# Performance work log

Hardware: AMD Instinct MI355X
Metric: run time of the kernel (lower is better)

Reference implementation:

```python
import jax, jax.numpy as jnp
import numpy as np

B, T, C = 2, 2048, 1024
H = 16
D = C // H  # head_dim = 64
EPS = 1e-06
MAX_SEQ = 2048


def make_rotary(dim, max_seq_len, base=10000):
    inv_freq = 1.0 / (base ** (jnp.arange(0, dim, 2, dtype=jnp.float32) / dim))
    pos = jnp.arange(max_seq_len, dtype=jnp.float32)
    sinusoid = jnp.einsum('i,j->ij', pos, inv_freq)  # (S, dim//2)
    return jnp.sin(sinusoid), jnp.cos(sinusoid)


def apply_rotary(x, sin, cos):
    # x: (B, T, H, D); sin/cos: (MAX_SEQ, D//2)
    t = x.shape[1]
    s = sin[:t][:, None, :]  # (T,1,D//2) broadcasts over B and H
    c = cos[:t][:, None, :]
    d = x.shape[-1]
    x1, x2 = x[..., :d // 2], x[..., d // 2:]
    return jnp.concatenate([x1 * c - x2 * s, x2 * c + x1 * s], axis=-1)


def yat_dense(x, kernel, bias, alpha, eps=EPS):
    # Yat layer: squared dot product over squared euclidean distance.
    dot = x @ kernel                                   # (..., out)
    x_sq = jnp.sum(x * x, axis=-1, keepdims=True)      # (..., 1)
    k_sq = jnp.sum(kernel * kernel, axis=0)            # (out,)
    dist = x_sq + k_sq - 2.0 * dot
    y = (dot * dot) / (dist + eps)
    out_f = kernel.shape[1]
    scale = (jnp.sqrt(jnp.float32(out_f)) / jnp.log(1.0 + jnp.float32(out_f))) ** alpha
    return y * scale + bias


def setup_inputs() -> dict:
    key = jax.random.key(0)
    ks = jax.random.split(key, 7)
    x = jax.random.normal(ks[0], (B, T, C), dtype=jnp.float32)
    mask = jnp.tril(jnp.ones((T, T), dtype=bool))[None].repeat(B, axis=0)  # (B,T,T) causal
    s = 1.0 / np.sqrt(C)
    w_attn = jax.random.normal(ks[1], (C, 3 * C), dtype=jnp.float32) * s
    b_attn = jnp.zeros((3 * C,), dtype=jnp.float32)
    a_attn = jnp.ones((1,), dtype=jnp.float32)
    w_proj = jax.random.normal(ks[2], (C, C), dtype=jnp.float32) * s
    b_proj = jnp.zeros((C,), dtype=jnp.float32)
    a_proj = jnp.ones((1,), dtype=jnp.float32)
    return {"x": x, "mask": mask, "w_attn": w_attn, "b_attn": b_attn,
            "a_attn": a_attn, "w_proj": w_proj, "b_proj": b_proj, "a_proj": a_proj}


def reference(x, mask, w_attn, b_attn, a_attn, w_proj, b_proj, a_proj):
    b, t, c = x.shape
    sin, cos = make_rotary(D, MAX_SEQ)
    qkv = yat_dense(x, w_attn, b_attn, a_attn)          # (B,T,3C)
    qkv = qkv.reshape(b, t, 3, H, D)
    q, k, v = jnp.moveaxis(qkv, 2, 0)                   # each (B,T,H,D)
    q = apply_rotary(q, sin, cos)
    k = apply_rotary(k, sin, cos)
    # heads-major layout for attention
    q = q.transpose(0, 2, 1, 3)                          # (B,H,T,D)
    k = k.transpose(0, 2, 1, 3)
    v = v.transpose(0, 2, 1, 3)
    scale = jnp.sqrt(jnp.float32(D))
    attn = jnp.einsum('bhqd,bhkd->bhqk', q, k) / scale   # (B,H,T,T)
    m = mask[:, None, :, :]                              # (B,1,T,T)
    attn = jnp.where(m, attn, jnp.finfo(jnp.float32).min)
    attn = jax.nn.softmax(attn, axis=-1)
    # dropout is identity in deterministic/eval mode
    out = jnp.einsum('bhqk,bhkd->bhqd', attn, v)         # (B,H,T,D)
    out = out.transpose(0, 2, 1, 3).reshape(b, t, c)     # (B,T,C)
    out = yat_dense(out, w_proj, b_proj, a_proj)
    return out
```

## Files before the change

### kernel.cpp

```cpp
#include <hip/hip_runtime.h>
#include <math.h>

#define TSEQ  2048
#define BATCH 2
#define NH    16
#define HD    64
#define CDIM  1024
#define N3C   3072
#define EPSY  1e-6f

typedef unsigned short u16;
typedef unsigned int u32;
typedef __attribute__((ext_vector_type(2))) unsigned int u32x2;
typedef __attribute__((ext_vector_type(8))) short bf16x8;
typedef __attribute__((ext_vector_type(4))) float f32x4;

#define MFMA16(a, b, c) __builtin_amdgcn_mfma_f32_16x16x32_bf16(a, b, c, 0, 0, 0)

__device__ __forceinline__ u16 f2bf(float f) {
    unsigned u = __float_as_uint(f);
    return (u16)((u + 0x7fffu + ((u >> 16) & 1u)) >> 16);
}
__device__ __forceinline__ u32 cvtpk_bf16(float lo, float hi) {
    u32 r;
    asm("v_cvt_pk_bf16_f32 %0, %1, %2" : "=v"(r) : "v"(lo), "v"(hi));
    return r;
}
__device__ __forceinline__ void gload16(const void* g, void* l) {
    __builtin_amdgcn_global_load_lds(
        (const __attribute__((address_space(1))) unsigned int*)g,
        (__attribute__((address_space(3))) unsigned int*)l, 16, 0, 0);
}

__global__ __launch_bounds__(256) void prep_kernel(
    const float* __restrict__ x, const float* __restrict__ wa,
    const float* __restrict__ wp, u16* __restrict__ Ahi,
    u16* __restrict__ Wthi, u16* __restrict__ Wphi,
    float* __restrict__ ksq, float* __restrict__ xsq,
    float* __restrict__ osq, float2* __restrict__ ropeSC) {
    __shared__ float smem[64 * 68];
    int bid = blockIdx.x, tid = threadIdx.x;

    if (bid < 4096) {
        int lane = tid & 63, wv = tid >> 6;
        size_t base = (size_t)bid * CDIM + tid * 4;
        float4 v = *(const float4*)(x + base);
        ushort4 hi;
        hi.x = f2bf(v.x); hi.y = f2bf(v.y); hi.z = f2bf(v.z); hi.w = f2bf(v.w);
        *(ushort4*)(Ahi + base) = hi;
        float s = v.x * v.x + v.y * v.y + v.z * v.z + v.w * v.w;
        #pragma unroll
        for (int off = 32; off; off >>= 1) s += __shfl_down(s, off, 64);
        if (lane == 0) smem[wv] = s;
        __syncthreads();
        if (tid == 0) xsq[bid] = smem[0] + smem[1] + smem[2] + smem[3];
    } else if (bid < 5120) {
        const float* W; u16* Whi; int K, N, bx, by;
        if (bid < 4864) {
            int t = bid - 4096; W = wa; Whi = Wthi; K = CDIM; N = N3C;
            bx = t % 48; by = t / 48;
        } else {
            int t = bid - 4864; W = wp; Whi = Wphi; K = CDIM; N = CDIM;
            bx = t % 16; by = t / 16;
        }
        int k0 = by * 64, n0 = bx * 64;
        int r = tid >> 4, c4 = (tid & 15) * 4;
        #pragma unroll
        for (int i = 0; i < 4; ++i) {
            int k = k0 + r + i * 16;
            float4 v = *(const float4*)(W + (size_t)k * N + n0 + c4);
            *(float4*)&smem[(r + i * 16) * 68 + c4] = v;
        }
        __syncthreads();
        int n = tid >> 4, k4 = (tid & 15) * 4;
        #pragma unroll
        for (int i = 0; i < 4; ++i) {
            int nn = n + i * 16;
            ushort4 hi;
            hi.x = f2bf(smem[(k4 + 0) * 68 + nn]);
            hi.y = f2bf(smem[(k4 + 1) * 68 + nn]);
            hi.z = f2bf(smem[(k4 + 2) * 68 + nn]);
            hi.w = f2bf(smem[(k4 + 3) * 68 + nn]);
            *(ushort4*)(Whi + (size_t)(n0 + nn) * K + k0 + k4) = hi;
        }
    } else if (bid < 5184) {
        int b2 = bid - 5120;
        int c = tid & 63, kq = tid >> 6;
        const float* W; int N, col, outoff;
        if (b2 < 48) { W = wa; N = N3C;  col = b2 * 64 + c;        outoff = 0;   }
        else         { W = wp; N = CDIM; col = (b2 - 48) * 64 + c; outoff = N3C; }
        float s = 0.f;
        int i0 = kq * 256;
        #pragma unroll 4
        for (int i = i0; i < i0 + 256; ++i) {
            float v = W[(size_t)i * N + col];
            s = fmaf(v, v, s);
        }
        smem[tid] = s;
        __syncthreads();
        if (kq == 0)
            ksq[outoff + col] = smem[c] + smem[64 + c] + smem[128 + c] + smem[192 + c];
    } else {
        int idx = (bid - 5184) * 256 + tid;
        if (idx < BATCH * TSEQ) osq[idx] = 0.f;
        int t = idx >> 5, j = idx & 31;
        float inv = exp2f(-(float)j * 0.4152410118609203f);
        float ang = (float)t * inv;
        ropeSC[idx] = make_float2(cosf(ang), sinf(ang));
    }
}

__global__ __launch_bounds__(256, 4) void gemm1_fused(
    const u16* __restrict__ Ah, const u16* __restrict__ Bh,
    const float* __restrict__ bias, const float* __restrict__ rowsq,
    const float* __restrict__ colsq, const float* __restrict__ alphap,
    const float2* __restrict__ ropeSC,
    u16* __restrict__ Qb, u16* __restrict__ Kb, u16* __restrict__ Vt) {
    constexpr int BK = 32;
    const int K = CDIM;
    __shared__ u16 Ash[2][128 * BK], Bsh[2][128 * BK];
    int tid = threadIdx.x;
    int lane = tid & 63, wv = tid >> 6;
    int quad = lane >> 4, l15 = lane & 15;
    int wr = wv >> 1, wc = wv & 1;

    int lin = blockIdx.x + blockIdx.y * 24;
    int swz = (lin & 7) * 96 + (lin >> 3);
    int bn = (swz % 24) * 128;
    int bm = (swz / 24) * 128;

    int rsub = lane >> 2;
    int lc8 = (lane & 3) * 8;
    int gc8 = (((lane & 3) - (rsub >> 1)) & 3) * 8;
    int pf8 = ((quad + (l15 >> 1)) & 3) * 8;

    f32x4 acc[4][4];
    #pragma unroll
    for (int i = 0; i < 4; ++i)
        #pragma unroll
        for (int j = 0; j < 4; ++j) acc[i][j] = (f32x4){0.f, 0.f, 0.f, 0.f};

    auto STAGE = [&](int buf, int kt) {
        #pragma unroll
        for (int i = 0; i < 2; ++i) {
            int r = i * 64 + wv * 16 + rsub;
            gload16(Ah + (size_t)(bm + r) * K + kt + gc8, &Ash[buf][r * BK + lc8]);
            gload16(Bh + (size_t)(bn + r) * K + kt + gc8, &Bsh[buf][r * BK + lc8]);
        }
    };

    STAGE(0, 0);
    __syncthreads();
    int cur = 0;

    for (int kt = 0; kt < K; kt += BK) {
        if (kt + BK < K) STAGE(cur ^ 1, kt + BK);
        bf16x8 fah[4], fbh[4];
        #pragma unroll
        for (int i = 0; i < 4; ++i)
            fah[i] = *(const bf16x8*)&Ash[cur][(wr * 64 + i * 16 + l15) * BK + pf8];
        #pragma unroll
        for (int j = 0; j < 4; ++j)
            fbh[j] = *(const bf16x8*)&Bsh[cur][(wc * 64 + j * 16 + l15) * BK + pf8];
        #pragma unroll
        for (int i = 0; i < 4; ++i)
            #pragma unroll
            for (int j = 0; j < 4; ++j)
                acc[i][j] = MFMA16(fah[i], fbh[j], acc[i][j]);
        __syncthreads();
        cur ^= 1;
    }

    float alpha = alphap[0];
    float scale = powf(sqrtf((float)N3C) / logf(1.0f + (float)N3C), alpha);
    int segc0 = bn + wc * 64;
    int seg = segc0 >> 10;
    int h = (segc0 >> 6) & 15;
    int bglob = bm >> 11;
    int bh = bglob * NH + h;

    if (seg < 2) {
        u16* dst = (seg == 0) ? Qb : Kb;
        float qs = (seg == 0) ? 0.18033688011112043f : 1.0f;
        #pragma unroll
        for (int i = 0; i < 4; ++i) {
            int tb = bm + wr * 64 + i * 16 + quad * 4;
            #pragma unroll
            for (int r = 0; r < 4; ++r) {
                int row = tb + r;
                int t = row & (TSEQ - 1);
                float rs = rowsq[row];
                float y[4];
                #pragma unroll
                for (int j = 0; j < 4; ++j) {
                    int col = segc0 + j * 16 + l15;
                    float dot = acc[i][j][r];
                    float dist = rs + colsq[col] - 2.0f * dot + EPSY;
                    y[j] = dot * dot / dist * scale + bias[col];
                }
                float2 sc0 = ropeSC[t * 32 + l15];
                float2 sc1 = ropeSC[t * 32 + 16 + l15];
                float c0 = sc0.x, s0 = sc0.y, c1 = sc1.x, s1 = sc1.y;
                size_t ob = ((size_t)bh * TSEQ + t) * HD;
                dst[ob + l15]      = f2bf((y[0] * c0 - y[2] * s0) * qs);
                dst[ob + 16 + l15] = f2bf((y[1] * c1 - y[3] * s1) * qs);
                dst[ob + 32 + l15] = f2bf((y[2] * c0 + y[0] * s0) * qs);
                dst[ob + 48 + l15] = f2bf((y[3] * c1 + y[1] * s1) * qs);
            }
        }
    } else {
        #pragma unroll
        for (int i = 0; i < 4; ++i) {
            int tb = bm + wr * 64 + i * 16 + quad * 4;
            int t0 = tb & (TSEQ - 1);
            #pragma unroll
            for (int j = 0; j < 4; ++j) {
                int col = segc0 + j * 16 + l15;
                int d = j * 16 + l15;
                float cs = colsq[col], bi = bias[col];
                ushort4 pk;
                u16* pp = (u16*)&pk;
                #pragma unroll
                for (int r = 0; r < 4; ++r) {
                    float dot = acc[i][j][r];
                    float dist = rowsq[tb + r] + cs - 2.0f * dot + EPSY;
                    pp[r] = f2bf(dot * dot / dist * scale + bi);
                }
                *(ushort4*)(Vt + ((size_t)bh * HD + d) * TSEQ + t0) = pk;
            }
        }
    }
}

__global__ __launch_bounds__(128, 4) void gemm_yat_mfma(
    const u16* __restrict__ Ah, const u16* __restrict__ Bh,
    const float* __restrict__ bias, const float* __restrict__ rowsq,
    const float* __restrict__ colsq, const float* __restrict__ alphap,
    float* __restrict__ outp, int M, int N, int K, float outf) {
    constexpr int BM = 64, BN = 64, BK = 32;
    __shared__ u16 Ash[2][BM * BK], Bsh[2][BN * BK];
    int tid = threadIdx.x;
    int lane = tid & 63, wv = tid >> 6;
    int quad = lane >> 4, l15 = lane & 15;

    int lin = blockIdx.x + blockIdx.y * 16;
    int swz = (lin & 7) * 128 + (lin >> 3);
    int bn = (swz & 15) * BN;
    int bm = (swz >> 4) * BM;

    int rs = tid >> 2;
    int cc = tid & 3;
    int lc8 = cc * 8;
    int gc8 = ((cc - ((rs & 15) >> 1)) & 3) * 8;
    int pf8 = ((quad + (l15 >> 1)) & 3) * 8;

    f32x4 acc[2][4];
    #pragma unroll
    for (int i = 0; i < 2; ++i)
        #pragma unroll
        for (int j = 0; j < 4; ++j) acc[i][j] = (f32x4){0.f, 0.f, 0.f, 0.f};

    auto STAGE = [&](int buf, int kt) {
        #pragma unroll
        for (int p = 0; p < 2; ++p) {
            int r = p * 32 + rs;
            gload16(Ah + (size_t)(bm + r) * K + kt + gc8, &Ash[buf][r * BK + lc8]);
            gload16(Bh + (size_t)(bn + r) * K + kt + gc8, &Bsh[buf][r * BK + lc8]);
        }
    };

    STAGE(0, 0);
    __syncthreads();
    int cur = 0;

    for (int kt = 0; kt < K; kt += BK) {
        if (kt + BK < K) STAGE(cur ^ 1, kt + BK);
        bf16x8 fah[2], fbh[4];
        #pragma unroll
        for (int i = 0; i < 2; ++i)
            fah[i] = *(const bf16x8*)&Ash[cur][(wv * 32 + i * 16 + l15) * BK + pf8];
        #pragma unroll
        for (int j = 0; j < 4; ++j)
            fbh[j] = *(const bf16x8*)&Bsh[cur][(j * 16 + l15) * BK + pf8];
        #pragma unroll
        for (int i = 0; i < 2; ++i)
            #pragma unroll
            for (int j = 0; j < 4; ++j)
                acc[i][j] = MFMA16(fah[i], fbh[j], acc[i][j]);
        __syncthreads();
        cur ^= 1;
    }

    float alpha = alphap[0];
    float scale = powf(sqrtf(outf) / logf(1.0f + outf), alpha);
    #pragma unroll
    for (int j = 0; j < 4; ++j) {
        int col = bn + j * 16 + l15;
        float cs = colsq[col], bi = bias[col];
        #pragma unroll
        for (int i = 0; i < 2; ++i) {
            #pragma unroll
            for (int r = 0; r < 4; ++r) {
                int row = bm + wv * 32 + i * 16 + quad * 4 + r;
                float dot = acc[i][j][r];
                float dist = rowsq[row] + cs - 2.0f * dot + EPSY;
                outp[(size_t)row * N + col] = dot * dot / dist * scale + bi;
            }
        }
    }
}

__global__ __launch_bounds__(512) void attn_mfma(
    const u16* __restrict__ Qb, const u16* __restrict__ Kb,
    const u16* __restrict__ Vt, u16* __restrict__ Chi,
    float* __restrict__ osq) {
    __shared__ u16 Ksh[2][64 * 64];
    __shared__ u16 Vsh[2][64 * 64];
    int tid = threadIdx.x;
    int lane = tid & 63, wv = tid >> 6;
    int quad = lane >> 4, l15 = lane & 15;
    const bool oddq = (quad & 1) != 0;
    int bh = blockIdx.x;
    int b = bh >> 4, h = bh & 15;
    const u16* Qh = Qb + (size_t)bh * TSEQ * HD;
    const u16* Kh = Kb + (size_t)bh * TSEQ * HD;
    const u16* Vh = Vt + (size_t)bh * HD * TSEQ;
    const f32x4 zf = {0.f, 0.f, 0.f, 0.f};

    int qbb = 15 - blockIdx.y;
    int qw = qbb * 128 + wv * 16;
    int NT = 2 * qbb + 2;
    bf16x8 bq0 = *(const bf16x8*)(Qh + (size_t)(qw + l15) * HD + quad * 8);
    bf16x8 bq1 = *(const bf16x8*)(Qh + (size_t)(qw + l15) * HD + 32 + quad * 8);

    f32x4 o[4] = {zf, zf, zf, zf};
    float l = 0.f;

    auto STAGE = [&](int buf, int kt) {
        int k0s = kt * 64;
        int rowi = tid >> 3, ch = tid & 7;
        int gk = (ch + rowi) & 7;
        gload16(Kh + (size_t)(k0s + rowi) * HD + gk * 8, &Ksh[buf][tid * 8]);
        gload16(Vh + (size_t)rowi * TSEQ + k0s + gk * 8, &Vsh[buf][tid * 8]);
    };

    STAGE(0, 0);
    __syncthreads();
    int cur = 0;

    for (int kt = 0; kt < NT; ++kt) {
        int k0 = kt * 64;
        if (kt + 1 < NT) STAGE(cur ^ 1, kt + 1);
        if (k0 <= qw + 15) {
            const u16* Kc = Ksh[cur];
            const u16* Vc = Vsh[cur];

            f32x4 st[4];
            __builtin_amdgcn_s_setprio(1);
            #pragma unroll
            for (int mt = 0; mt < 4; ++mt) {
                int key = mt * 16 + l15;
                bf16x8 a0 = *(const bf16x8*)&Kc[key * 64 + ((quad - key) & 7) * 8];
                bf16x8 a1 = *(const bf16x8*)&Kc[key * 64 + ((4 + quad - key) & 7) * 8];
                st[mt] = MFMA16(a0, bq0, zf);
                st[mt] = MFMA16(a1, bq1, st[mt]);
            }
            __builtin_amdgcn_s_setprio(0);
            if (k0 + 63 > qw) {
                int q = qw + l15;
                #pragma unroll
                for (int mt = 0; mt < 4; ++mt)
                    #pragma unroll
                    for (int r = 0; r < 4; ++r)
                        if (k0 + mt * 16 + quad * 4 + r > q) st[mt][r] = -1e30f;
            }
            u32 pp[4][2];
            #pragma unroll
            for (int mt = 0; mt < 4; ++mt) {
                float p0 = __builtin_amdgcn_exp2f(st[mt][0]);
                float p1 = __builtin_amdgcn_exp2f(st[mt][1]);
                float p2 = __builtin_amdgcn_exp2f(st[mt][2]);
                float p3 = __builtin_amdgcn_exp2f(st[mt][3]);
                l += (p0 + p1) + (p2 + p3);
                pp[mt][0] = cvtpk_bf16(p0, p1);
                pp[mt][1] = cvtpk_bf16(p2, p3);
            }
            #pragma unroll
            for (int s = 0; s < 2; ++s) {
                u32x2 r0 = __builtin_amdgcn_permlane32_swap(
                    pp[2 * s][0], pp[2 * s + 1][0], false, false);
                u32 sA0 = (u32)__builtin_amdgcn_ds_swizzle((int)r0.x, 0x401F);
                u32 sB0 = (u32)__builtin_amdgcn_ds_swizzle((int)r0.y, 0x401F);
                u32x2 r1 = __builtin_amdgcn_permlane32_swap(
                    pp[2 * s][1], pp[2 * s + 1][1], false, false);
                u32 sA1 = (u32)__builtin_amdgcn_ds_swizzle((int)r1.x, 0x401F);
                u32 sB1 = (u32)__builtin_amdgcn_ds_swizzle((int)r1.y, 0x401F);
                u32 bw0 = oddq ? sB0 : r0.x;
                u32 bw1 = oddq ? sB1 : r1.x;
                u32 bw2 = oddq ? r0.y : sA0;
                u32 bw3 = oddq ? r1.y : sA1;
                bf16x8 bfr;
                *(u32*)&((short*)&bfr)[0] = bw0;
                *(u32*)&((short*)&bfr)[2] = bw1;
                *(u32*)&((short*)&bfr)[4] = bw2;
                *(u32*)&((short*)&bfr)[6] = bw3;
                __builtin_amdgcn_s_setprio(1);
                #pragma unroll
                for (int dt = 0; dt < 4; ++dt) {
                    int d = dt * 16 + l15;
                    bf16x8 av = *(const bf16x8*)&Vc[d * 64 + ((s * 4 + quad - d) & 7) * 8];
                    o[dt] = MFMA16(av, bfr, o[dt]);
                }
                __builtin_amdgcn_s_setprio(0);
            }
        }
        __syncthreads();
        cur ^= 1;
    }

    l += __shfl_xor(l, 16, 64);
    l += __shfl_xor(l, 32, 64);
    float inv = 1.0f / l;
    int row = (b << 11) + qw + l15;
    float ss = 0.f;
    #pragma unroll
    for (int dt = 0; dt < 4; ++dt) {
        float v0 = o[dt][0] * inv, v1 = o[dt][1] * inv;
        float v2 = o[dt][2] * inv, v3 = o[dt][3] * inv;
        ss += v0 * v0 + v1 * v1 + v2 * v2 + v3 * v3;
        uint2 pk2;
        pk2.x = cvtpk_bf16(v0, v1);
        pk2.y = cvtpk_bf16(v2, v3);
        *(uint2*)(Chi + (size_t)row * CDIM + h * HD + dt * 16 + quad * 4) = pk2;
    }
    ss += __shfl_xor(ss, 16, 64);
    ss += __shfl_xor(ss, 32, 64);
    if (quad == 0) atomicAdd(osq + row, ss);
}

extern "C" void kernel_launch(void* const* d_in, const int* in_sizes, int n_in,
                              void* d_out, int out_size, void* d_ws, size_t ws_size,
                              hipStream_t stream) {
    const float* x      = (const float*)d_in[0];
    const float* w_attn = (const float*)d_in[2];
    const float* b_attn = (const float*)d_in[3];
    const float* a_attn = (const float*)d_in[4];
    const float* w_proj = (const float*)d_in[5];
    const float* b_proj = (const float*)d_in[6];
    const float* a_proj = (const float*)d_in[7];
    float* outp = (float*)d_out;

    char* ws = (char*)d_ws;
    float* ksq = (float*)(ws);
    float* xsq = (float*)(ws + 16384);
    float* osq = (float*)(ws + 32768);
    char* pA  = ws + 65536;
    u16* Ahi = (u16*)pA;
    u16* Chi = (u16*)pA;
    char* pWt = pA + 16777216;
    u16* Wthi = (u16*)pWt;
    char* pWp = pWt + 6291456;
    u16* Wphi = (u16*)pWp;
    char* pQ = pWp + 2097152;
    u16* Qb = (u16*)pQ;
    u16* Kb = (u16*)(pQ + 8388608);
    u16* Vt = (u16*)(pQ + 16777216);
    float2* ropeSC = (float2*)(pQ + 25165824);

    prep_kernel<<<5440, 256, 0, stream>>>(
        x, w_attn, w_proj, Ahi, Wthi, Wphi, ksq, xsq, osq, ropeSC);
    gemm1_fused<<<dim3(N3C / 128, (BATCH * TSEQ) / 128), 256, 0, stream>>>(
        Ahi, Wthi, b_attn, xsq, ksq, a_attn, ropeSC, Qb, Kb, Vt);
    attn_mfma<<<dim3(BATCH * NH, 16), 512, 0, stream>>>(Qb, Kb, Vt, Chi, osq);
    gemm_yat_mfma<<<dim3(CDIM / 64, (BATCH * TSEQ) / 64), 128, 0, stream>>>(
        Chi, Wphi, b_proj, osq, ksq + N3C, a_proj, outp,
        BATCH * TSEQ, CDIM, CDIM, (float)CDIM);
}
```

Measured before the change: 222.8 us.

## Drop LDS staging in attention, read K/V directly from global memory

The attention kernel no longer stages K and V tiles through double-buffered shared memory with block-wide barriers. Each wave now loads its MFMA operands for K and V straight from global memory, relying on L1/L2 caches. Blocks shrink from 8 waves covering 128 query rows to 4 waves covering 64 rows, and the grid doubles so causal work is spread more finely. This removes the barriers and the LDS traffic, but each wave now fetches K/V on its own with uncoalesced, cache-dependent loads and loses cross-wave reuse.

```diff
diff --git a/kernel.cpp b/kernel.cpp
--- a/kernel.cpp
+++ b/kernel.cpp
@@ -310,12 +310,10 @@
     }
 }
 
-__global__ __launch_bounds__(512) void attn_mfma(
+__global__ __launch_bounds__(256) void attn_mfma(
     const u16* __restrict__ Qb, const u16* __restrict__ Kb,
     const u16* __restrict__ Vt, u16* __restrict__ Chi,
     float* __restrict__ osq) {
-    __shared__ u16 Ksh[2][64 * 64];
-    __shared__ u16 Vsh[2][64 * 64];
     int tid = threadIdx.x;
     int lane = tid & 63, wv = tid >> 6;
     int quad = lane >> 4, l15 = lane & 15;
@@ -327,95 +325,78 @@
     const u16* Vh = Vt + (size_t)bh * HD * TSEQ;
     const f32x4 zf = {0.f, 0.f, 0.f, 0.f};
 
-    int qbb = 15 - blockIdx.y;
-    int qw = qbb * 128 + wv * 16;
-    int NT = 2 * qbb + 2;
+    int qblk = 31 - blockIdx.y;
+    int qw = qblk * 64 + wv * 16;
+    int NT = qblk + 1;
     bf16x8 bq0 = *(const bf16x8*)(Qh + (size_t)(qw + l15) * HD + quad * 8);
     bf16x8 bq1 = *(const bf16x8*)(Qh + (size_t)(qw + l15) * HD + 32 + quad * 8);
 
     f32x4 o[4] = {zf, zf, zf, zf};
     float l = 0.f;
 
-    auto STAGE = [&](int buf, int kt) {
-        int k0s = kt * 64;
-        int rowi = tid >> 3, ch = tid & 7;
-        int gk = (ch + rowi) & 7;
-        gload16(Kh + (size_t)(k0s + rowi) * HD + gk * 8, &Ksh[buf][tid * 8]);
-        gload16(Vh + (size_t)rowi * TSEQ + k0s + gk * 8, &Vsh[buf][tid * 8]);
-    };
-
-    STAGE(0, 0);
-    __syncthreads();
-    int cur = 0;
-
     for (int kt = 0; kt < NT; ++kt) {
         int k0 = kt * 64;
-        if (kt + 1 < NT) STAGE(cur ^ 1, kt + 1);
-        if (k0 <= qw + 15) {
-            const u16* Kc = Ksh[cur];
-            const u16* Vc = Vsh[cur];
-
-            f32x4 st[4];
+        if (k0 > qw + 15) continue;
+
+        f32x4 st[4];
+        __builtin_amdgcn_s_setprio(1);
+        #pragma unroll
+        for (int mt = 0; mt < 4; ++mt) {
+            int key = k0 + mt * 16 + l15;
+            const u16* kr = Kh + (size_t)key * HD;
+            bf16x8 a0 = *(const bf16x8*)(kr + quad * 8);
+            bf16x8 a1 = *(const bf16x8*)(kr + 32 + quad * 8);
+            st[mt] = MFMA16(a0, bq0, zf);
+            st[mt] = MFMA16(a1, bq1, st[mt]);
+        }
+        __builtin_amdgcn_s_setprio(0);
+        if (k0 + 63 > qw) {
+            int q = qw + l15;
+            #pragma unroll
+            for (int mt = 0; mt < 4; ++mt)
+                #pragma unroll
+                for (int r = 0; r < 4; ++r)
+                    if (k0 + mt * 16 + quad * 4 + r > q) st[mt][r] = -1e30f;
+        }
+        u32 pp[4][2];
+        #pragma unroll
+        for (int mt = 0; mt < 4; ++mt) {
+            float p0 = __builtin_amdgcn_exp2f(st[mt][0]);
+            float p1 = __builtin_amdgcn_exp2f(st[mt][1]);
+            float p2 = __builtin_amdgcn_exp2f(st[mt][2]);
+            float p3 = __builtin_amdgcn_exp2f(st[mt][3]);
+            l += (p0 + p1) + (p2 + p3);
+            pp[mt][0] = cvtpk_bf16(p0, p1);
+            pp[mt][1] = cvtpk_bf16(p2, p3);
+        }
+        #pragma unroll
+        for (int s = 0; s < 2; ++s) {
+            u32x2 r0 = __builtin_amdgcn_permlane32_swap(
+                pp[2 * s][0], pp[2 * s + 1][0], false, false);
+            u32 sA0 = (u32)__builtin_amdgcn_ds_swizzle((int)r0.x, 0x401F);
+            u32 sB0 = (u32)__builtin_amdgcn_ds_swizzle((int)r0.y, 0x401F);
+            u32x2 r1 = __builtin_amdgcn_permlane32_swap(
+                pp[2 * s][1], pp[2 * s + 1][1], false, false);
+            u32 sA1 = (u32)__builtin_amdgcn_ds_swizzle((int)r1.x, 0x401F);
+            u32 sB1 = (u32)__builtin_amdgcn_ds_swizzle((int)r1.y, 0x401F);
+            u32 bw0 = oddq ? sB0 : r0.x;
+            u32 bw1 = oddq ? sB1 : r1.x;
+            u32 bw2 = oddq ? r0.y : sA0;
+            u32 bw3 = oddq ? r1.y : sA1;
+            bf16x8 bfr;
+            *(u32*)&((short*)&bfr)[0] = bw0;
+            *(u32*)&((short*)&bfr)[2] = bw1;
+            *(u32*)&((short*)&bfr)[4] = bw2;
+            *(u32*)&((short*)&bfr)[6] = bw3;
             __builtin_amdgcn_s_setprio(1);
             #pragma unroll
-            for (int mt = 0; mt < 4; ++mt) {
-                int key = mt * 16 + l15;
-                bf16x8 a0 = *(const bf16x8*)&Kc[key * 64 + ((quad - key) & 7) * 8];
-                bf16x8 a1 = *(const bf16x8*)&Kc[key * 64 + ((4 + quad - key) & 7) * 8];
-                st[mt] = MFMA16(a0, bq0, zf);
-                st[mt] = MFMA16(a1, bq1, st[mt]);
+            for (int dt = 0; dt < 4; ++dt) {
+                int d = dt * 16 + l15;
+                bf16x8 av = *(const bf16x8*)(Vh + (size_t)d * TSEQ + k0 + (s * 4 + quad) * 8);
+                o[dt] = MFMA16(av, bfr, o[dt]);
             }
             __builtin_amdgcn_s_setprio(0);
-            if (k0 + 63 > qw) {
-                int q = qw + l15;
-                #pragma unroll
-                for (int mt = 0; mt < 4; ++mt)
-                    #pragma unroll
-                    for (int r = 0; r < 4; ++r)
-                        if (k0 + mt * 16 + quad * 4 + r > q) st[mt][r] = -1e30f;
-            }
-            u32 pp[4][2];
-            #pragma unroll
-            for (int mt = 0; mt < 4; ++mt) {
-                float p0 = __builtin_amdgcn_exp2f(st[mt][0]);
-                float p1 = __builtin_amdgcn_exp2f(st[mt][1]);
-                float p2 = __builtin_amdgcn_exp2f(st[mt][2]);
-                float p3 = __builtin_amdgcn_exp2f(st[mt][3]);
-                l += (p0 + p1) + (p2 + p3);
-                pp[mt][0] = cvtpk_bf16(p0, p1);
-                pp[mt][1] = cvtpk_bf16(p2, p3);
-            }
-            #pragma unroll
-            for (int s = 0; s < 2; ++s) {
-                u32x2 r0 = __builtin_amdgcn_permlane32_swap(
-                    pp[2 * s][0], pp[2 * s + 1][0], false, false);
-                u32 sA0 = (u32)__builtin_amdgcn_ds_swizzle((int)r0.x, 0x401F);
-                u32 sB0 = (u32)__builtin_amdgcn_ds_swizzle((int)r0.y, 0x401F);
-                u32x2 r1 = __builtin_amdgcn_permlane32_swap(
-                    pp[2 * s][1], pp[2 * s + 1][1], false, false);
-                u32 sA1 = (u32)__builtin_amdgcn_ds_swizzle((int)r1.x, 0x401F);
-                u32 sB1 = (u32)__builtin_amdgcn_ds_swizzle((int)r1.y, 0x401F);
-                u32 bw0 = oddq ? sB0 : r0.x;
-                u32 bw1 = oddq ? sB1 : r1.x;
-                u32 bw2 = oddq ? r0.y : sA0;
-                u32 bw3 = oddq ? r1.y : sA1;
-                bf16x8 bfr;
-                *(u32*)&((short*)&bfr)[0] = bw0;
-                *(u32*)&((short*)&bfr)[2] = bw1;
-                *(u32*)&((short*)&bfr)[4] = bw2;
-                *(u32*)&((short*)&bfr)[6] = bw3;
-                __builtin_amdgcn_s_setprio(1);
-                #pragma unroll
-                for (int dt = 0; dt < 4; ++dt) {
-                    int d = dt * 16 + l15;
-                    bf16x8 av = *(const bf16x8*)&Vc[d * 64 + ((s * 4 + quad - d) & 7) * 8];
-                    o[dt] = MFMA16(av, bfr, o[dt]);
-                }
-                __builtin_amdgcn_s_setprio(0);
-            }
-        }
-        __syncthreads();
-        cur ^= 1;
+        }
     }
 
     l += __shfl_xor(l, 16, 64);
@@ -471,7 +452,7 @@
         x, w_attn, w_proj, Ahi, Wthi, Wphi, ksq, xsq, osq, ropeSC);
     gemm1_fused<<<dim3(N3C / 128, (BATCH * TSEQ) / 128), 256, 0, stream>>>(
         Ahi, Wthi, b_attn, xsq, ksq, a_attn, ropeSC, Qb, Kb, Vt);
-    attn_mfma<<<dim3(BATCH * NH, 16), 512, 0, stream>>>(Qb, Kb, Vt, Chi, osq);
+    attn_mfma<<<dim3(BATCH * NH, 32), 256, 0, stream>>>(Qb, Kb, Vt, Chi, osq);
     gemm_yat_mfma<<<dim3(CDIM / 64, (BATCH * TSEQ) / 64), 128, 0, stream>>>(
         Chi, Wphi, b_proj, osq, ksq + N3C, a_proj, outp,
         BATCH * TSEQ, CDIM, CDIM, (float)CDIM);
```

Measured after the change: 326.7 us. +46.6%, slower.
